# Kernel optimization log

Hardware: AMD Instinct MI355X
Metric: run time of the kernel (lower is better)

## Reference

```python
import jax, jax.numpy as jnp
import numpy as np

NUM_CLASSES = 2   # module init num_classes; class logits have NUM_CLASSES+1 (incl. 'no object')
ORIG_H, ORIG_W = 512, 512  # original input resolution that masks are upsampled to


def setup_inputs() -> dict:
    key = jax.random.key(0)
    k1, k2 = jax.random.split(key)
    B, Q = 8, 100
    h, w = 128, 128  # mask decoder outputs at 1/4 input resolution
    class_queries_logits = jax.random.normal(k1, (B, Q, NUM_CLASSES + 1), dtype=jnp.float32)
    masks_queries_logits = jax.random.normal(k2, (B, Q, h, w), dtype=jnp.float32)
    return {"class_queries_logits": class_queries_logits,
            "masks_queries_logits": masks_queries_logits}


def reference(class_queries_logits, masks_queries_logits):
    B, Q = masks_queries_logits.shape[:2]
    # bilinear upsample to original resolution (align_corners=False == half-pixel centers)
    masks_up = jax.image.resize(masks_queries_logits, (B, Q, ORIG_H, ORIG_W), method="bilinear")
    # softmax over classes (incl. no-object), keep only the first NUM_CLASSES,
    # exactly as the original loop only indexes c in range(num_classes)
    class_probs = jax.nn.softmax(class_queries_logits, axis=-1)[..., :NUM_CLASSES]  # [B,Q,C]
    mask_probs = jax.nn.sigmoid(masks_up)  # [B,Q,H,W]
    # fused replacement for the triple b/q/c Python loop of weighted accumulates
    logits = jnp.einsum("bqc,bqhw->bchw", class_probs, mask_probs)  # [B,C,H,W]
    return logits
```

## Files before the change

### kernel.cpp

```cpp
#include <hip/hip_runtime.h>
#include <math.h>

#define NB 8
#define NQ 100
#define NCP1 3
#define NC 2
#define HIN 128
#define WIN 128
#define HOUT 512
#define WOUT 512
#define QSTR (HIN * WIN)

#if __has_builtin(__builtin_amdgcn_exp2f)
#define EXP2F(x) __builtin_amdgcn_exp2f(x)
#else
#define EXP2F(x) exp2f(x)
#endif
#if __has_builtin(__builtin_amdgcn_rcpf)
#define RCPF(x) __builtin_amdgcn_rcpf(x)
#else
#define RCPF(x) (1.0f / (x))
#endif

__device__ __forceinline__ float bperm(int byteaddr, float v) {
  return __int_as_float(__builtin_amdgcn_ds_bpermute(byteaddr, __float_as_int(v)));
}

__global__ __launch_bounds__(256, 4)
void m2f_fused(const float* __restrict__ cls,
               const float* __restrict__ masks,
               float* __restrict__ out) {
  const int k   = blockIdx.x;
  const int b   = blockIdx.y;
  const int tid = threadIdx.x;

  __shared__ float2 pq[NQ];

  if (tid < NQ) {
    const float* cl = cls + (b * NQ + tid) * NCP1;
    float a0 = cl[0], a1 = cl[1], a2 = cl[2];
    float mx = fmaxf(a0, fmaxf(a1, a2));
    const float L2E = 1.4426950408889634f;
    float e0 = EXP2F((a0 - mx) * L2E);
    float e1 = EXP2F((a1 - mx) * L2E);
    float e2 = EXP2F((a2 - mx) * L2E);
    float inv = RCPF(e0 + e1 + e2);
    pq[tid] = make_float2(e0 * inv, e1 * inv);
  }
  __syncthreads();

  const int r    = tid >> 6;
  const int lane = tid & 63;

  const int rlo = (r < 2) ? (k > 0 ? k - 1 : 0) : k;
  const int rhi = (r < 2) ? k : (k < HIN - 1 ? k + 1 : HIN - 1);
  const float NL2E = -1.4426950408889634f;
  const float wlo = ((r == 0) ? 0.375f : (r == 1) ? 0.125f
                   : (r == 2) ? 0.875f : 0.625f) * NL2E;
  const float whi = ((r == 0) ? 0.625f : (r == 1) ? 0.875f
                   : (r == 2) ? 0.125f : 0.375f) * NL2E;

  const int oA = rlo * WIN + 2 * lane;
  const int oB = rhi * WIN + 2 * lane;
  const float* __restrict__ base = masks + (size_t)b * NQ * QSTR;

  const int addrL = (lane - 1) << 2;
  const int addrR = (lane + 1) << 2;
  const bool edgeL = (lane == 0);
  const bool edgeR = (lane == 63);

  float c0[8], c1[8];
#pragma unroll
  for (int j = 0; j < 8; ++j) { c0[j] = 0.f; c1[j] = 0.f; }

  float2 A0, B0, A1, B1, A2, B2, A3, B3;

#define LOADSET(S, qq)                                                    \
  do {                                                                    \
    const float* mq = base + (size_t)(qq) * QSTR;   \
    A##S = *(const float2*)(mq + oA);                                     \
    B##S = *(const float2*)(mq + oB);                                     \
  } while (0)

#define COMPUTE(S, qq)                                                    \
  do {                                                                    \
    const float2 pd = pq[qq];                                             \
            \
    float t0 = fmaf(wlo, A##S.x, whi * B##S.x);             \
    float t1 = fmaf(wlo, A##S.y, whi * B##S.y);             \
    \
    float tLr = bperm(addrL, t1);                                         \
    float tRr = bperm(addrR, t0);                                         \
    float tL = edgeL ? t0 : tLr;                                          \
    float tR = edgeR ? t1 : tRr;                                          \
                                          \
    float dm = tL - t0, dd = t1 - t0, dp = tR - t1;                       \
    float v0 = fmaf(0.375f, dm, t0);                                      \
    float v1 = fmaf(0.125f, dm, t0);                                      \
    float v2 = fmaf(0.125f, dd, t0);                                      \
    float v3 = fmaf(0.375f, dd, t0);                                      \
    float v4 = fmaf(0.625f, dd, t0);                                      \
    float v5 = fmaf(0.875f, dd, t0);                                      \
    float v6 = fmaf(0.125f, dp, t1);                                      \
    float v7 = fmaf(0.375f, dp, t1);                                      \
       \
    float s0 = RCPF(1.0f + EXP2F(v0));                                    \
    float s1 = RCPF(1.0f + EXP2F(v1));                                    \
    float s2 = RCPF(1.0f + EXP2F(v2));                                    \
    float s3 = RCPF(1.0f + EXP2F(v3));                                    \
    float s4 = RCPF(1.0f + EXP2F(v4));                                    \
    float s5 = RCPF(1.0f + EXP2F(v5));                                    \
    float s6 = RCPF(1.0f + EXP2F(v6));                                    \
    float s7 = RCPF(1.0f + EXP2F(v7));                                    \
    c0[0] = fmaf(pd.x, s0, c0[0]);  c1[0] = fmaf(pd.y, s0, c1[0]);        \
    c0[1] = fmaf(pd.x, s1, c0[1]);  c1[1] = fmaf(pd.y, s1, c1[1]);        \
    c0[2] = fmaf(pd.x, s2, c0[2]);  c1[2] = fmaf(pd.y, s2, c1[2]);        \
    c0[3] = fmaf(pd.x, s3, c0[3]);  c1[3] = fmaf(pd.y, s3, c1[3]);        \
    c0[4] = fmaf(pd.x, s4, c0[4]);  c1[4] = fmaf(pd.y, s4, c1[4]);        \
    c0[5] = fmaf(pd.x, s5, c0[5]);  c1[5] = fmaf(pd.y, s5, c1[5]);        \
    c0[6] = fmaf(pd.x, s6, c0[6]);  c1[6] = fmaf(pd.y, s6, c1[6]);        \
    c0[7] = fmaf(pd.x, s7, c0[7]);  c1[7] = fmaf(pd.y, s7, c1[7]);        \
  } while (0)

  LOADSET(0, 0); LOADSET(1, 1); LOADSET(2, 2); LOADSET(3, 3);

  for (int q = 0; q < NQ; q += 4) {
    COMPUTE(0, q);     if (q + 4 < NQ) LOADSET(0, q + 4);
    COMPUTE(1, q + 1); if (q + 5 < NQ) LOADSET(1, q + 5);
    COMPUTE(2, q + 2); if (q + 6 < NQ) LOADSET(2, q + 6);
    COMPUTE(3, q + 3); if (q + 7 < NQ) LOADSET(3, q + 7);
  }

  const int y  = 4 * k + r;
  const int x0 = 8 * lane;
  float* o0 = out + (((size_t)b * NC + 0) * HOUT + y) * WOUT + x0;
  float* o1 = out + (((size_t)b * NC + 1) * HOUT + y) * WOUT + x0;
  *(float4*)o0       = make_float4(c0[0], c0[1], c0[2], c0[3]);
  *(float4*)(o0 + 4) = make_float4(c0[4], c0[5], c0[6], c0[7]);
  *(float4*)o1       = make_float4(c1[0], c1[1], c1[2], c1[3]);
  *(float4*)(o1 + 4) = make_float4(c1[4], c1[5], c1[6], c1[7]);
}

extern "C" void kernel_launch(void* const* d_in, const int* in_sizes, int n_in,
                              void* d_out, int out_size, void* d_ws, size_t ws_size,
                              hipStream_t stream) {
  const float* cls   = (const float*)d_in[0];
  const float* masks = (const float*)d_in[1];
  float* out = (float*)d_out;
  dim3 grid(HIN, NB);
  m2f_fused<<<grid, 256, 0, stream>>>(cls, masks, out);
}
```

Baseline: 138.1 us.

## Split query loop across two wave groups with shared-memory reduction

Doubles the block to 512 threads so two groups of four waves each handle half of the 100 queries for the same output rows. The partial sums from the second group go through a 16x256 shared-memory buffer and are added by the first group before it stores. This is meant to shorten the serial per-thread query loop and raise the number of waves in flight to hide latency. It costs extra shared memory, a block-wide barrier and a reduction step, and the higher launch bound may limit registers.

After: 255.7 us. +85.1%, slower.

```diff
diff --git a/kernel.cpp b/kernel.cpp
--- a/kernel.cpp
+++ b/kernel.cpp
@@ -3,6 +3,7 @@
 
 #define NB 8
 #define NQ 100
+#define NQH 50
 #define NCP1 3
 #define NC 2
 #define HIN 128
@@ -26,7 +27,7 @@
   return __int_as_float(__builtin_amdgcn_ds_bpermute(byteaddr, __float_as_int(v)));
 }
 
-__global__ __launch_bounds__(256, 4)
+__global__ __launch_bounds__(512, 8)
 void m2f_fused(const float* __restrict__ cls,
                const float* __restrict__ masks,
                float* __restrict__ out) {
@@ -35,6 +36,7 @@
   const int tid = threadIdx.x;
 
   __shared__ float2 pq[NQ];
+  __shared__ float  part[16][256];
 
   if (tid < NQ) {
     const float* cl = cls + (b * NQ + tid) * NCP1;
@@ -49,8 +51,11 @@
   }
   __syncthreads();
 
-  const int r    = tid >> 6;
+  const int wave = tid >> 6;
+  const int r    = wave & 3;
+  const int qh   = wave >> 2;
   const int lane = tid & 63;
+  const int q0   = qh * NQH;
 
   const int rlo = (r < 2) ? (k > 0 ? k - 1 : 0) : k;
   const int rhi = (r < 2) ? k : (k < HIN - 1 ? k + 1 : HIN - 1);
@@ -85,15 +90,12 @@
 #define COMPUTE(S, qq)                                                    \
   do {                                                                    \
     const float2 pd = pq[qq];                                             \
-            \
     float t0 = fmaf(wlo, A##S.x, whi * B##S.x);             \
     float t1 = fmaf(wlo, A##S.y, whi * B##S.y);             \
-    \
     float tLr = bperm(addrL, t1);                                         \
     float tRr = bperm(addrR, t0);                                         \
     float tL = edgeL ? t0 : tLr;                                          \
     float tR = edgeR ? t1 : tRr;                                          \
-                                          \
     float dm = tL - t0, dd = t1 - t0, dp = tR - t1;                       \
     float v0 = fmaf(0.375f, dm, t0);                                      \
     float v1 = fmaf(0.125f, dm, t0);                                      \
@@ -103,7 +105,6 @@
     float v5 = fmaf(0.875f, dd, t0);                                      \
     float v6 = fmaf(0.125f, dp, t1);                                      \
     float v7 = fmaf(0.375f, dp, t1);                                      \
-       \
     float s0 = RCPF(1.0f + EXP2F(v0));                                    \
     float s1 = RCPF(1.0f + EXP2F(v1));                                    \
     float s2 = RCPF(1.0f + EXP2F(v2));                                    \
@@ -122,23 +123,36 @@
     c0[7] = fmaf(pd.x, s7, c0[7]);  c1[7] = fmaf(pd.y, s7, c1[7]);        \
   } while (0)
 
-  LOADSET(0, 0); LOADSET(1, 1); LOADSET(2, 2); LOADSET(3, 3);
+  LOADSET(0, q0); LOADSET(1, q0 + 1); LOADSET(2, q0 + 2); LOADSET(3, q0 + 3);
 
-  for (int q = 0; q < NQ; q += 4) {
-    COMPUTE(0, q);     if (q + 4 < NQ) LOADSET(0, q + 4);
-    COMPUTE(1, q + 1); if (q + 5 < NQ) LOADSET(1, q + 5);
-    COMPUTE(2, q + 2); if (q + 6 < NQ) LOADSET(2, q + 6);
-    COMPUTE(3, q + 3); if (q + 7 < NQ) LOADSET(3, q + 7);
+  for (int q = 0; q < NQH - 2; q += 4) {
+    COMPUTE(0, q0 + q);     if (q + 4 < NQH) LOADSET(0, q0 + q + 4);
+    COMPUTE(1, q0 + q + 1); if (q + 5 < NQH) LOADSET(1, q0 + q + 5);
+    COMPUTE(2, q0 + q + 2); if (q + 6 < NQH) LOADSET(2, q0 + q + 6);
+    COMPUTE(3, q0 + q + 3); if (q + 7 < NQH) LOADSET(3, q0 + q + 7);
   }
+  COMPUTE(0, q0 + NQH - 2);
+  COMPUTE(1, q0 + NQH - 1);
 
-  const int y  = 4 * k + r;
-  const int x0 = 8 * lane;
-  float* o0 = out + (((size_t)b * NC + 0) * HOUT + y) * WOUT + x0;
-  float* o1 = out + (((size_t)b * NC + 1) * HOUT + y) * WOUT + x0;
-  *(float4*)o0       = make_float4(c0[0], c0[1], c0[2], c0[3]);
-  *(float4*)(o0 + 4) = make_float4(c0[4], c0[5], c0[6], c0[7]);
-  *(float4*)o1       = make_float4(c1[0], c1[1], c1[2], c1[3]);
-  *(float4*)(o1 + 4) = make_float4(c1[4], c1[5], c1[6], c1[7]);
+  const int col = r * 64 + lane;
+  if (qh == 1) {
+#pragma unroll
+    for (int j = 0; j < 8; ++j) { part[j][col] = c0[j]; part[j + 8][col] = c1[j]; }
+  }
+  __syncthreads();
+  if (qh == 0) {
+#pragma unroll
+    for (int j = 0; j < 8; ++j) { c0[j] += part[j][col]; c1[j] += part[j + 8][col]; }
+
+    const int y  = 4 * k + r;
+    const int x0 = 8 * lane;
+    float* o0 = out + (((size_t)b * NC + 0) * HOUT + y) * WOUT + x0;
+    float* o1 = out + (((size_t)b * NC + 1) * HOUT + y) * WOUT + x0;
+    *(float4*)o0       = make_float4(c0[0], c0[1], c0[2], c0[3]);
+    *(float4*)(o0 + 4) = make_float4(c0[4], c0[5], c0[6], c0[7]);
+    *(float4*)o1       = make_float4(c1[0], c1[1], c1[2], c1[3]);
+    *(float4*)(o1 + 4) = make_float4(c1[4], c1[5], c1[6], c1[7]);
+  }
 }
 
 extern "C" void kernel_launch(void* const* d_in, const int* in_sizes, int n_in,
@@ -148,5 +162,5 @@
   const float* masks = (const float*)d_in[1];
   float* out = (float*)d_out;
   dim3 grid(HIN, NB);
-  m2f_fused<<<grid, 256, 0, stream>>>(cls, masks, out);
+  m2f_fused<<<grid, 512, 0, stream>>>(cls, masks, out);
 }
```
